# Kernel optimization log

Measured on AMD Instinct MI355X. Metric: run time of the kernel, lower is better.

## Reference

```python
import jax, jax.numpy as jnp
import numpy as np

CR = 64                      # cond_repeat
DILS = tuple(2 ** i for _ in range(2) for i in range(10))  # 2 blocks x 10 layers
Q_ZERO = 128


def setup_inputs() -> dict:
    key = jax.random.key(0)
    B, C, TE = 8, 64, 8          # batch, cond channels, encoding timesteps
    R, S, Q = 128, 128, 256      # residual, skip, classes
    L = len(DILS)
    ks = jax.random.split(key, 12)
    sc = 0.1
    return {
        "encodings": jax.random.normal(ks[0], (B, C, TE), jnp.float32),
        "first_w": jax.random.normal(ks[1], (R, 1, 2), jnp.float32) * sc,
        "first_b": jnp.zeros((R,), jnp.float32),
        "causal_w": jax.random.normal(ks[2], (L, 2 * R, R, 2), jnp.float32) * sc,
        "causal_b": jnp.zeros((L, 2 * R), jnp.float32),
        "cond_w": jax.random.normal(ks[3], (L, 2 * R, C), jnp.float32) * sc,
        "cond_b": jnp.zeros((L, 2 * R), jnp.float32),
        "res_w": jax.random.normal(ks[4], (L, R, R), jnp.float32) * sc,
        "res_b": jnp.zeros((L, R), jnp.float32),
        "skip_w": jax.random.normal(ks[5], (L, S, R), jnp.float32) * sc,
        "skip_b": jnp.zeros((L, S), jnp.float32),
        "skipc_w": jax.random.normal(ks[6], (S, R), jnp.float32) * sc,
        "skipc_b": jnp.zeros((S,), jnp.float32),
        "fc_w": jax.random.normal(ks[7], (S, S), jnp.float32) * sc,
        "fc_b": jnp.zeros((S,), jnp.float32),
        "condf_w": jax.random.normal(ks[8], (S, C), jnp.float32) * sc,
        "condf_b": jnp.zeros((S,), jnp.float32),
        "logits_w": jax.random.normal(ks[9], (Q, S), jnp.float32) * sc,
        "logits_b": jnp.zeros((Q,), jnp.float32),
    }


def _generate(encodings, first_w, first_b, causal_w, causal_b, cond_w, cond_b,
              res_w, res_b, skip_w, skip_b, skipc_w, skipc_b, fc_w, fc_b,
              condf_w, condf_b, logits_w, logits_b):
    B = encodings.shape[0]
    R = res_w.shape[1]
    T = encodings.shape[2] * CR

    # ring buffers emulate QueuedConv1d (queue length = dilation, zero-initialized)
    buf_first0 = jnp.zeros((B, 1), jnp.float32)
    bufs0 = tuple(jnp.zeros((B, d, R), jnp.float32) for d in DILS)
    sample0 = jnp.full((B,), Q_ZERO, jnp.int32)

    def step(carry, t):
        sample, buf_first, bufs = carry
        x = sample.astype(jnp.float32) / 255.0 - 0.5                      # [B]
        c = jax.lax.dynamic_index_in_dim(encodings, t // CR, axis=2,
                                         keepdims=False)                  # [B,C]
        # first causal conv (1 -> R, kernel 2): tap0 on delayed sample, tap1 on current
        prev0 = buf_first[:, 0]
        buf_first = buf_first.at[:, 0].set(x)
        res = (prev0[:, None] * first_w[None, :, 0, 0]
               + x[:, None] * first_w[None, :, 0, 1] + first_b)           # [B,R]
        skip = res @ skipc_w.T + skipc_b                                  # [B,S]
        new_bufs = []
        for l, d in enumerate(DILS):
            idx = jnp.mod(t, d)
            prev = jax.lax.dynamic_index_in_dim(bufs[l], idx, axis=1, keepdims=False)
            new_bufs.append(jax.lax.dynamic_update_index_in_dim(bufs[l], res, idx, axis=1))
            z = (prev @ causal_w[l, :, :, 0].T + res @ causal_w[l, :, :, 1].T
                 + causal_b[l] + c @ cond_w[l].T + cond_b[l])             # [B,2R]
            gate, out = jnp.split(z, 2, axis=1)
            h = jax.nn.sigmoid(gate) * jnp.tanh(out)                      # [B,R]
            res = res + h @ res_w[l].T + res_b[l]
            skip = skip + h @ skip_w[l].T + skip_b[l]
        s = jax.nn.relu(skip) @ fc_w.T + fc_b + c @ condf_w.T + condf_b
        logits = jax.nn.relu(s) @ logits_w.T + logits_b                   # [B,Q]
        sample = jnp.argmax(logits, axis=1).astype(jnp.int32)             # 'max' sampling
        return (sample, buf_first, tuple(new_bufs)), (sample, logits)

    _, (samples, logits) = jax.lax.scan(step, (sample0, buf_first0, bufs0),
                                        jnp.arange(T))
    return samples, logits  # [T,B] int32, [T,B,Q] float32


def reference(encodings, first_w, first_b, causal_w, causal_b, cond_w, cond_b,
              res_w, res_b, skip_w, skip_b, skipc_w, skipc_b, fc_w, fc_b,
              condf_w, condf_b, logits_w, logits_b):
    return _generate(encodings, first_w, first_b, causal_w, causal_b, cond_w, cond_b,
                     res_w, res_b, skip_w, skip_b, skipc_w, skipc_b, fc_w, fc_b,
                     condf_w, condf_b, logits_w, logits_b)
```

## Files before the change

### kernel.cpp

```cpp
#include <hip/hip_runtime.h>
#include <math.h>

#define BB 8
#define TT 512
#define LL 20
#define NBLK 64
#define NTHR 256

typedef float f4 __attribute__((ext_vector_type(4)));
typedef unsigned long long ull;

__constant__ int c_dil[LL] = {1,2,4,8,16,32,64,128,256,512,
                              1,2,4,8,16,32,64,128,256,512};
__constant__ int c_roff[LL] = {-1,0,4096,12288,28672,61440,126976,258048,520192,1044480,
                               2093056,2095104,2099200,2107392,2123776,2156544,
                               2222080,2353152,2615296,3139584};

constexpr size_t OFF_RING = 0;
constexpr size_t OFF_X    = 4188160;

#define P_WC     0
#define P_F      20480
#define P_WST    30208
#define P_WSKIPC 30720
#define P_WFC    30976
#define P_WLOG   31232
#define P_WF0    31744
#define P_WF1    31872
#define P_FB     32000
#define P_CONDZ  32128
#define P_SFC    32768
#define P_RESB   32784
#define P_SKIPB  32824
#define P_ZB     32864
#define P_LOGB   32944
#define P_SKIPCB 32948
#define P_Z0C    32952
#define P_SKC    32976
#define P_XS     32984
#define P_SZ     33008
#define P_SL     33040
#define P_SKACC  33072
#define P_R2     33088
#define P_CF     33104
#define P_PREVF  33632
#define P_HF     34688
#define P_RESF   35744
#define P_RES0   36800
#define POOL_FL  37856

__device__ __forceinline__ f4 ldx(const f4* p) {
    f4 r;
    asm volatile("global_load_dwordx4 %0, %1, off sc0 sc1\n\ts_waitcnt vmcnt(0)"
                 : "=v"(r) : "v"(p) : "memory");
    return r;
}
__device__ __forceinline__ void ldx2(const f4* p0, const f4* p1, f4& a, f4& b) {
    asm volatile("global_load_dwordx4 %0, %2, off sc0 sc1\n\t"
                 "global_load_dwordx4 %1, %3, off sc0 sc1\n\t"
                 "s_waitcnt vmcnt(0)"
                 : "=v"(a), "=v"(b) : "v"(p0), "v"(p1) : "memory");
}
__device__ __forceinline__ void ld4x(const f4* a0, const f4* a1, const f4* a2, const f4* a3,
                                     f4& r0, f4& r1, f4& r2, f4& r3) {
    asm volatile("global_load_dwordx4 %0, %4, off sc0 sc1\n\t"
                 "global_load_dwordx4 %1, %5, off sc0 sc1\n\t"
                 "global_load_dwordx4 %2, %6, off sc0 sc1\n\t"
                 "global_load_dwordx4 %3, %7, off sc0 sc1\n\t"
                 "s_waitcnt vmcnt(0)"
                 : "=v"(r0), "=v"(r1), "=v"(r2), "=v"(r3)
                 : "v"(a0), "v"(a1), "v"(a2), "v"(a3) : "memory");
}
__device__ __forceinline__ void stx(f4* p, f4 v) {
    asm volatile("global_store_dwordx4 %0, %1, off sc0 sc1"
                 :: "v"(p), "v"(v) : "memory");
}
__device__ __forceinline__ void spin(const f4* p, int e, f4& a) {
    while (__float_as_int(a.w) != e) a = ldx(p);
}

__device__ __forceinline__ float pick16(const float* sl, int V) {
    if (V < 8) return sl[V];
    if (V >= 9 && V < 17) return sl[V - 1];
    return 0.f;
}
__device__ __forceinline__ void publish16(f4* slot, int J, const float* sl, int e) {
    if (threadIdx.x < 6) {
        int q = threadIdx.x;
        f4 v;
        v.x = pick16(sl, 3*q);
        v.y = pick16(sl, 3*q + 1);
        v.z = pick16(sl, 3*q + 2);
        v.w = __int_as_float(e);
        stx(slot + J*6 + q, v);
    }
}
__device__ __forceinline__ void publish_half(f4* slot, int J, int r, const float* half8,
                                             int e, int m) {
    int base = 3*m;
    f4 v;
    v.x = half8[base];
    v.y = (base + 1 < 8) ? half8[base + 1] : 0.f;
    v.z = (base + 2 < 8) ? half8[base + 2] : 0.f;
    v.w = __int_as_float(e);
    stx(slot + J*6 + 3*r + m, v);
}
__device__ __forceinline__ void scat16(float* dst, f4 v, int vi, bool dorelu) {
    int j = vi / 6, q = vi - 6*j;
    #pragma unroll
    for (int i = 0; i < 3; ++i) {
        int V = 3*q + i;
        float x = v[i];
        if (dorelu) x = fmaxf(x, 0.f);
        if (V < 8)                 dst[V*132 + 2*j]           = x;
        else if (V >= 9 && V < 17) dst[(V - 9)*132 + 2*j + 1] = x;
    }
}
__device__ __forceinline__ void consume16(const f4* slot, int e, float* dst, bool dorelu) {
    int m = threadIdx.x;
    const f4 *p0 = slot + m, *p1 = slot + 256 + m;
    f4 a, b;
    bool two = (m < 128);
    if (two) ldx2(p0, p1, a, b); else a = ldx(p0);
    spin(p0, e, a);
    if (two) spin(p1, e, b);
    scat16(dst, a, m, dorelu);
    if (two) scat16(dst, b, m + 256, dorelu);
}
__device__ __forceinline__ void consume_pair(const f4* sR, int eR, float* dR,
                                             const f4* sH, int eH, float* dH) {
    int m = threadIdx.x;
    const f4 *pra = sR + m, *prb = sR + 256 + m, *pha = sH + m, *phb = sH + 256 + m;
    f4 ra, rb, ha, hb;
    bool two = (m < 128);
    if (two) ld4x(pra, prb, pha, phb, ra, rb, ha, hb);
    else     ldx2(pra, pha, ra, ha);
    spin(pra, eR, ra);
    if (two) spin(prb, eR, rb);
    scat16(dR, ra, m, false);
    if (two) scat16(dR, rb, m + 256, false);
    spin(pha, eH, ha);
    if (two) spin(phb, eH, hb);
    scat16(dH, ha, m, false);
    if (two) scat16(dH, hb, m + 256, false);
}

__global__ __launch_bounds__(NTHR, 1) void wn_gen(
    const float* __restrict__ enc,
    const float* __restrict__ first_w,  const float* __restrict__ first_b,
    const float* __restrict__ causal_w, const float* __restrict__ causal_b,
    const float* __restrict__ cond_w,   const float* __restrict__ cond_b,
    const float* __restrict__ res_w,    const float* __restrict__ res_b,
    const float* __restrict__ skip_w,   const float* __restrict__ skip_b,
    const float* __restrict__ skipc_w,  const float* __restrict__ skipc_b,
    const float* __restrict__ fc_w,     const float* __restrict__ fc_b,
    const float* __restrict__ condf_w,  const float* __restrict__ condf_b,
    const float* __restrict__ logits_w, const float* __restrict__ logits_b,
    float* __restrict__ wsf, float* __restrict__ out)
{
    extern __shared__ float pool[];
    const int tid = threadIdx.x;
    const int J = blockIdx.x;
    float* ring = wsf + OFF_RING;
    f4* xb = (f4*)(wsf + OFF_X);

    for (int m = tid; m < 20480; m += NTHR) {
        int l = m >> 10, rem = m & 1023, g = rem >> 8, i = rem & 255;
        int grow = (g < 2) ? (2*J + g) : (128 + 2*J + (g - 2));
        int col = i & 127, k = i >> 7;
        pool[P_WC + m] = causal_w[((size_t)(l*256 + grow)*128 + col)*2 + k];
    }
    if (tid < 256) {
        int r = tid >> 7, i = tid & 127;
        pool[P_WSKIPC + tid] = skipc_w[(size_t)(2*J + r)*128 + i];
        pool[P_WFC + tid]    = fc_w[(size_t)(2*J + r)*128 + i];
    }
    for (int m = tid; m < 512; m += NTHR) {
        int w = m >> 7, i = m & 127;
        pool[P_WLOG + m] = logits_w[(size_t)(4*J + w)*128 + i];
    }
    if (tid < 128) {
        pool[P_WF0 + tid] = first_w[2*tid];
        pool[P_WF1 + tid] = first_w[2*tid + 1];
        pool[P_FB + tid]  = first_b[tid];
    }
    if (tid < 40) {
        int l = tid >> 1, r = tid & 1;
        pool[P_RESB + tid]  = res_b[l*128 + 2*J + r];
        pool[P_SKIPB + tid] = skip_b[l*128 + 2*J + r];
    }
    if (tid < 4) pool[P_LOGB + tid] = logits_b[4*J + tid];
    if (tid < 2) pool[P_SKIPCB + tid] = skipc_b[2*J + tid];
    if (tid < 8) {
        pool[P_XS + tid]      = 128.f/255.f - 0.5f;
        pool[P_XS + 8 + tid]  = 0.f;
        pool[P_XS + 16 + tid] = 0.f;
    }
    __syncthreads();

    for (int l = 0; l < 19; ++l) {
        for (int m = tid; m < 512; m += NTHR) {
            int g = m >> 7, j = m & 127;
            const float* w1 = pool + P_WC + ((l+1)*4 + g)*256 + 128;
            const float* rw = res_w + (size_t)l*128*128 + j;
            float acc = 0.f;
            #pragma unroll 8
            for (int i = 0; i < 128; ++i) acc += w1[i] * rw[(size_t)i*128];
            pool[P_F + (l*4 + g)*128 + j] = acc;
        }
    }
    if (tid < 80) {
        int l = tid >> 2, g = tid & 3;
        float acc = 0.f;
        if (l >= 1) {
            const float* w1 = pool + P_WC + (l*4 + g)*256 + 128;
            for (int i = 0; i < 128; ++i) acc += w1[i] * res_b[(l-1)*128 + i];
        }
        pool[P_ZB + tid] = acc;
    }
    if (tid < 4) {
        const float* w0 = pool + P_WC + tid*256;
        const float* w1 = w0 + 128;
        float kp = 0.f, kc = 0.f, u = 0.f, c1 = 0.f, a0 = 0.f;
        for (int j = 0; j < 128; ++j) {
            float f0 = pool[P_WF0 + j], f1 = pool[P_WF1 + j], fbv = pool[P_FB + j];
            kp += w0[j]*fbv; kc += w1[j]*fbv;
            u  += w0[j]*f0;  c1 += w0[j]*f1 + w1[j]*f0;  a0 += w1[j]*f1;
        }
        pool[P_Z0C + tid*6 + 0] = kp;
        pool[P_Z0C + tid*6 + 1] = kc;
        pool[P_Z0C + tid*6 + 2] = u;
        pool[P_Z0C + tid*6 + 3] = c1;
        pool[P_Z0C + tid*6 + 4] = a0;
    }
    if (tid < 2) {
        const float* wr = pool + P_WSKIPC + tid*128;
        float sk = pool[P_SKIPCB + tid], sa = 0.f, sb = 0.f;
        for (int j = 0; j < 128; ++j) {
            sk += wr[j]*pool[P_FB + j];
            sa += wr[j]*pool[P_WF0 + j];
            sb += wr[j]*pool[P_WF1 + j];
        }
        pool[P_SKC + tid*3 + 0] = sk;
        pool[P_SKC + tid*3 + 1] = sa;
        pool[P_SKC + tid*3 + 2] = sb;
    }
    __syncthreads();

    int e = 0;
    int er_pending = 0;
    int esk = 0;

    for (int t = 0; t < TT; ++t) {
        if ((t & 63) == 0) {
            int te = t >> 6;
            for (int m = tid; m < 512; m += NTHR) {
                int b = m >> 6, j = m & 63;
                pool[P_CF + b*66 + j] = enc[(size_t)b*512 + j*8 + te];
            }
            __syncthreads();
            for (int m = tid; m < 640; m += NTHR) {
                int l = m >> 5, rem = m & 31, g = rem >> 3, b = rem & 7;
                int grow = (g < 2) ? (2*J + g) : (128 + 2*J + (g - 2));
                float acc = causal_b[l*256 + grow] + cond_b[l*256 + grow]
                          + pool[P_ZB + l*4 + g];
                const float* cw = cond_w + (size_t)(l*256 + grow)*64;
                const float* cf = pool + P_CF + b*66;
                for (int j = 0; j < 64; ++j) acc += cw[j]*cf[j];
                pool[P_CONDZ + l*32 + g*8 + b] = acc;
            }
            if (tid < 16) {
                int r = tid >> 3, b = tid & 7, row = 2*J + r;
                float acc = fc_b[row] + condf_b[row];
                const float* cw = condf_w + (size_t)row*64;
                const float* cf = pool + P_CF + b*66;
                for (int j = 0; j < 64; ++j) acc += cw[j]*cf[j];
                pool[P_SFC + r*8 + b] = acc;
            }
            __syncthreads();
        }

        ++e; const int eh0 = e;
        {
            if (tid < 16) {
                int r = tid & 1, b = tid >> 1;
                float kf  = (t >= 1) ? 1.f : 0.f;
                float x0v = pool[P_XS + b];
                float x1v = pool[P_XS + 8 + b];
                float x2v = pool[P_XS + 16 + b];
                const float* zc = pool + P_Z0C;
                int g0 = r, g1 = 2 + r;
                float zg = kf*zc[g0*6+0] + zc[g0*6+1] + x2v*zc[g0*6+2]
                         + x1v*zc[g0*6+3] + x0v*zc[g0*6+4] + pool[P_CONDZ + g0*8 + b];
                float zo = kf*zc[g1*6+0] + zc[g1*6+1] + x2v*zc[g1*6+2]
                         + x1v*zc[g1*6+3] + x0v*zc[g1*6+4] + pool[P_CONDZ + g1*8 + b];
                pool[P_SL + r*8 + b] = (1.f/(1.f + expf(-zg))) * tanhf(zo);
            }
            publish16(xb + (size_t)(eh0 & 3)*768, J, pool + P_SL, eh0);
        }
        for (int m = tid; m < 1024; m += NTHR) {
            int b = m >> 7, r = m & 127;
            pool[P_RES0 + b*132 + r] =
                pool[P_FB + r] + pool[P_XS + 8 + b]*pool[P_WF0 + r]
                               + pool[P_XS + b]    *pool[P_WF1 + r];
        }
        if (tid < 16) {
            int r = tid >> 3, b = tid & 7;
            float x0v = pool[P_XS + b], x1v = pool[P_XS + 8 + b];
            pool[P_SKACC + r*8 + b] = pool[P_SKC + r*3] + x1v*pool[P_SKC + r*3 + 1]
                                                        + x0v*pool[P_SKC + r*3 + 2];
            int row = 2*J + r;
            pool[P_R2 + r*8 + b] = pool[P_FB + row] + x1v*pool[P_WF0 + row]
                                                    + x0v*pool[P_WF1 + row];
        }

        for (int l = 0; l < LL; ++l) {
            int ehh;
            if (l == 0) {
                ehh = eh0;
            } else {
                {
                    int g = tid >> 6, lane = tid & 63, b = lane >> 3, k = lane & 7;
                    const float* w0 = pool + P_WC + (l*4 + g)*256;
                    const float* pv = pool + P_PREVF + b*132;
                    const float* rs = ((l == 1) ? pool + P_RES0 : pool + P_RESF) + b*132;
                    const float* fm = pool + P_F + ((l-1)*4 + g)*128;
                    const float* hh = pool + P_HF + b*132;
                    float acc = 0.f;
                    #pragma unroll
                    for (int i = 0; i < 16; ++i) {
                        int j = k + 8*i;
                        acc += w0[j]*pv[j] + w0[128 + j]*rs[j] + fm[j]*hh[j];
                    }
                    acc += __shfl_xor(acc,1); acc += __shfl_xor(acc,2); acc += __shfl_xor(acc,4);
                    if (k == 0) pool[P_SZ + g*8 + b] = acc;
                }
                __syncthreads();
                ++e; ehh = e;
                if (tid < 16) {
                    int r = tid & 1, b = tid >> 1;
                    float g = pool[P_SZ + r*8 + b]     + pool[P_CONDZ + l*32 + r*8 + b];
                    float o = pool[P_SZ + (2+r)*8 + b] + pool[P_CONDZ + l*32 + (2+r)*8 + b];
                    pool[P_SL + r*8 + b] = (1.f/(1.f + expf(-g))) * tanhf(o);
                }
                publish16(xb + (size_t)(ehh & 3)*768, J, pool + P_SL, ehh);
            }
            float wv0, wv1;
            {
                int r0 = tid >> 7, i0 = tid & 127;
                wv0 = res_w [(size_t)(l*128 + 2*J + r0)*128 + i0];
                wv1 = skip_w[(size_t)(l*128 + 2*J + r0)*128 + i0];
            }
            ull pfa = 0, pfb = 0;
            if (l <= 18) {
                int d = c_dil[l+1];
                if (t >= d) {
                    int slot = (t - d) & (2*d - 1);
                    const float* rp = ring + c_roff[l+1] + (size_t)slot*1024 + tid*4;
                    pfa = __hip_atomic_load((const ull*)rp,     __ATOMIC_RELAXED, __HIP_MEMORY_SCOPE_AGENT);
                    pfb = __hip_atomic_load((const ull*)(rp+2), __ATOMIC_RELAXED, __HIP_MEMORY_SCOPE_AGENT);
                }
            }
            if (l == 0) {
                consume16(xb + (size_t)(ehh & 3)*768, ehh, pool + P_HF, false);
            } else if (l <= 18) {
                consume_pair(xb + (size_t)(er_pending & 3)*768, er_pending, pool + P_RESF,
                             xb + (size_t)(ehh & 3)*768,        ehh,        pool + P_HF);
            } else {
                consume16(xb + (size_t)(ehh & 3)*768, ehh, pool + P_HF, false);
            }
            pool[P_WST + tid] = wv0;
            pool[P_WST + 256 + tid] = wv1;
            __syncthreads();
            {
                int w = tid >> 6, lane = tid & 63, b = lane >> 3, k = lane & 7;
                int r = w & 1, isSkip = w >> 1;
                if (isSkip || l <= 18) {
                    const float* wr = pool + P_WST + (isSkip ? 256 : 0) + r*128;
                    const float* hh = pool + P_HF + b*132;
                    float acc = 0.f;
                    #pragma unroll
                    for (int i = 0; i < 16; ++i) { int j = k + 8*i; acc += wr[j]*hh[j]; }
                    acc += __shfl_xor(acc,1); acc += __shfl_xor(acc,2); acc += __shfl_xor(acc,4);
                    if (k == 0) {
                        if (isSkip) {
                            pool[P_SKACC + r*8 + b] += acc + pool[P_SKIPB + l*2 + r];
                        } else {
                            float v = pool[P_R2 + r*8 + b] + acc + pool[P_RESB + l*2 + r];
                            pool[P_R2 + r*8 + b] = v;
                            pool[P_SL + r*8 + b] = v;
                            int d = c_dil[l+1];
                            int slot = t & (2*d - 1);
                            float* wp = ring + c_roff[l+1] + (size_t)slot*1024 + b*128 + 2*J + r;
                            __hip_atomic_store(wp, v, __ATOMIC_RELAXED, __HIP_MEMORY_SCOPE_AGENT);
                        }
                    }
                }
            }
            {
                int w = tid >> 6, lane = tid & 63;
                if (l <= 17) {
                    ++e; er_pending = e;
                    if (w < 2 && lane < 3)
                        publish_half(xb + (size_t)(e & 3)*768, J, w,
                                     pool + P_SL + w*8, e, lane);
                } else if (l == 19) {
                    ++e; esk = e;
                    if (w >= 2 && lane < 3)
                        publish_half(xb + (size_t)(e & 3)*768, J, w - 2,
                                     pool + P_SKACC + (w - 2)*8, e, lane);
                }
            }
            if (l <= 18) {
                int b = tid >> 5, c = (tid & 31)*4;
                union { ull u; float f[2]; } u0, u1;
                u0.u = pfa; u1.u = pfb;
                float* dp = pool + P_PREVF + b*132 + c;
                dp[0] = u0.f[0]; dp[1] = u0.f[1]; dp[2] = u1.f[0]; dp[3] = u1.f[1];
            }
            __syncthreads();
        }

        consume16(xb + (size_t)(esk & 3)*768, esk, pool + P_HF, false);
        __syncthreads();
        {
            int w = tid >> 6, lane = tid & 63, b = lane >> 3, k = lane & 7;
            if (w < 2) {
                const float* wr = pool + P_WFC + w*128;
                const float* sk = pool + P_HF + b*132;
                float acc = 0.f;
                #pragma unroll
                for (int i = 0; i < 16; ++i) { int j = k + 8*i; acc += wr[j]*fmaxf(sk[j], 0.f); }
                acc += __shfl_xor(acc,1); acc += __shfl_xor(acc,2); acc += __shfl_xor(acc,4);
                if (k == 0) pool[P_SL + w*8 + b] = acc + pool[P_SFC + w*8 + b];
            }
        }
        ++e;
        {
            int w = tid >> 6, lane = tid & 63;
            if (w < 2 && lane < 3)
                publish_half(xb + (size_t)(e & 3)*768, J, w, pool + P_SL + w*8, e, lane);
        }
        consume16(xb + (size_t)(e & 3)*768, e, pool + P_RESF, true);
        __syncthreads();
        {
            int b = tid >> 5, g = (tid >> 3) & 3, k = tid & 7;
            const float* wr = pool + P_WLOG + g*128;
            const float* sv = pool + P_RESF + b*132;
            float acc = 0.f;
            #pragma unroll
            for (int i = 0; i < 16; ++i) { int j = k + 8*i; acc += wr[j]*sv[j]; }
            acc += __shfl_xor(acc,1); acc += __shfl_xor(acc,2); acc += __shfl_xor(acc,4);
            float v = acc + pool[P_LOGB + g];
            float best = (k == 0) ? v : -3.4e38f;
            int bi = 4*J + g;
            { float ov = __shfl_xor(best, 8);  int oi = __shfl_xor(bi, 8);
              if (ov > best || (ov == best && oi < bi)) { best = ov; bi = oi; } }
            { float ov = __shfl_xor(best, 16); int oi = __shfl_xor(bi, 16);
              if (ov > best || (ov == best && oi < bi)) { best = ov; bi = oi; } }
            if (k == 0) out[4096 + ((size_t)(t*BB + b))*256 + 4*J + g] = v;
            if ((tid & 31) == 0) { pool[P_SL + b] = best; pool[P_SL + 8 + b] = (float)bi; }
        }
        __syncthreads();
        ++e;
        publish16(xb + (size_t)(e & 3)*768, J, pool + P_SL, e);
        consume16(xb + (size_t)(e & 3)*768, e, pool + P_HF, false);
        __syncthreads();
        if (tid < 64) {
            int b = tid >> 3, j0 = tid & 7;
            float best = -3.4e38f; float bidx = 0.f;
            #pragma unroll
            for (int k2 = 0; k2 < 8; ++k2) {
                int j = j0*8 + k2;
                float v  = pool[P_HF + b*132 + 2*j];
                float id = pool[P_HF + b*132 + 2*j + 1];
                if (v > best || (v == best && id < bidx)) { best = v; bidx = id; }
            }
            #pragma unroll
            for (int m = 4; m >= 1; m >>= 1) {
                float ov = __shfl_xor(best, m); float oi = __shfl_xor(bidx, m);
                if (ov > best || (ov == best && oi < bidx)) { best = ov; bidx = oi; }
            }
            if (j0 == 0) {
                if (J == 0) out[t*BB + b] = bidx;
                pool[P_XS + 16 + b] = pool[P_XS + 8 + b];
                pool[P_XS + 8 + b]  = pool[P_XS + b];
                pool[P_XS + b]      = bidx*(1.f/255.f) - 0.5f;
            }
        }
        __syncthreads();
    }
}

extern "C" void kernel_launch(void* const* d_in, const int* in_sizes, int n_in,
                              void* d_out, int out_size, void* d_ws, size_t ws_size,
                              hipStream_t stream) {
    const float* enc      = (const float*)d_in[0];
    const float* first_w  = (const float*)d_in[1];
    const float* first_b  = (const float*)d_in[2];
    const float* causal_w = (const float*)d_in[3];
    const float* causal_b = (const float*)d_in[4];
    const float* cond_w   = (const float*)d_in[5];
    const float* cond_b   = (const float*)d_in[6];
    const float* res_w    = (const float*)d_in[7];
    const float* res_b    = (const float*)d_in[8];
    const float* skip_w   = (const float*)d_in[9];
    const float* skip_b   = (const float*)d_in[10];
    const float* skipc_w  = (const float*)d_in[11];
    const float* skipc_b  = (const float*)d_in[12];
    const float* fc_w     = (const float*)d_in[13];
    const float* fc_b     = (const float*)d_in[14];
    const float* condf_w  = (const float*)d_in[15];
    const float* condf_b  = (const float*)d_in[16];
    const float* logits_w = (const float*)d_in[17];
    const float* logits_b = (const float*)d_in[18];

    float* wsf = (float*)d_ws;
    float* out = (float*)d_out;

    wn_gen<<<NBLK, NTHR, POOL_FL*4, stream>>>(
        enc, first_w, first_b, causal_w, causal_b, cond_w, cond_b,
        res_w, res_b, skip_w, skip_b, skipc_w, skipc_b, fc_w, fc_b,
        condf_w, condf_b, logits_w, logits_b, wsf, out);
}
```

Baseline: 35.99 ms.

## Compute layer-0 gate locally and fuse gate compute with publish to cut barriers

```diff
diff --git a/kernel.cpp b/kernel.cpp
--- a/kernel.cpp
+++ b/kernel.cpp
@@ -20,34 +20,30 @@
 constexpr size_t OFF_X    = 4188160;
 
 #define P_WC     0
+#define P_TB     0
 #define P_F      20480
-#define P_WST    30208
-#define P_WSKIPC 30720
-#define P_WFC    30976
-#define P_WLOG   31232
-#define P_WF0    31744
-#define P_WF1    31872
-#define P_FB     32000
-#define P_CONDZ  32128
-#define P_SFC    32768
-#define P_RESB   32784
-#define P_SKIPB  32824
-#define P_ZB     32864
-#define P_LOGB   32944
-#define P_SKIPCB 32948
-#define P_Z0C    32952
-#define P_SKC    32976
-#define P_XS     32984
-#define P_SZ     33008
-#define P_SL     33040
-#define P_SKACC  33072
-#define P_R2     33088
-#define P_CF     33104
-#define P_PREVF  33632
-#define P_HF     34688
-#define P_RESF   35744
-#define P_RES0   36800
-#define POOL_FL  37856
+#define P_CZ0    30208
+#define P_KC     32256
+#define P_WST    32512
+#define P_WF0    33024
+#define P_WF1    33152
+#define P_FB     33280
+#define P_CONDZ  33408
+#define P_SFC    34048
+#define P_RESB   34064
+#define P_SKIPB  34104
+#define P_ZB     34144
+#define P_LOGB   34224
+#define P_SKC    34228
+#define P_XS     34234
+#define P_SL     34258
+#define P_SKACC  34290
+#define P_R2     34306
+#define P_CF     34322
+#define P_PREVF  34852
+#define P_HF     35908
+#define P_RESF   38020
+#define POOL_FL  40132
 
 __device__ __forceinline__ f4 ldx(const f4* p) {
     f4 r;
@@ -59,7 +55,7 @@
     asm volatile("global_load_dwordx4 %0, %2, off sc0 sc1\n\t"
                  "global_load_dwordx4 %1, %3, off sc0 sc1\n\t"
                  "s_waitcnt vmcnt(0)"
-                 : "=v"(a), "=v"(b) : "v"(p0), "v"(p1) : "memory");
+                 : "=&v"(a), "=&v"(b) : "v"(p0), "v"(p1) : "memory");
 }
 __device__ __forceinline__ void ld4x(const f4* a0, const f4* a1, const f4* a2, const f4* a3,
                                      f4& r0, f4& r1, f4& r2, f4& r3) {
@@ -68,7 +64,7 @@
                  "global_load_dwordx4 %2, %6, off sc0 sc1\n\t"
                  "global_load_dwordx4 %3, %7, off sc0 sc1\n\t"
                  "s_waitcnt vmcnt(0)"
-                 : "=v"(r0), "=v"(r1), "=v"(r2), "=v"(r3)
+                 : "=&v"(r0), "=&v"(r1), "=&v"(r2), "=&v"(r3)
                  : "v"(a0), "v"(a1), "v"(a2), "v"(a3) : "memory");
 }
 __device__ __forceinline__ void stx(f4* p, f4 v) {
@@ -79,70 +75,46 @@
     while (__float_as_int(a.w) != e) a = ldx(p);
 }
 
-__device__ __forceinline__ float pick16(const float* sl, int V) {
-    if (V < 8) return sl[V];
-    if (V >= 9 && V < 17) return sl[V - 1];
-    return 0.f;
-}
-__device__ __forceinline__ void publish16(f4* slot, int J, const float* sl, int e) {
-    if (threadIdx.x < 6) {
-        int q = threadIdx.x;
-        f4 v;
-        v.x = pick16(sl, 3*q);
-        v.y = pick16(sl, 3*q + 1);
-        v.z = pick16(sl, 3*q + 2);
-        v.w = __int_as_float(e);
-        stx(slot + J*6 + q, v);
-    }
-}
-__device__ __forceinline__ void publish_half(f4* slot, int J, int r, const float* half8,
-                                             int e, int m) {
-    int base = 3*m;
-    f4 v;
-    v.x = half8[base];
-    v.y = (base + 1 < 8) ? half8[base + 1] : 0.f;
-    v.z = (base + 2 < 8) ? half8[base + 2] : 0.f;
-    v.w = __int_as_float(e);
-    stx(slot + J*6 + 3*r + m, v);
-}
-__device__ __forceinline__ void scat16(float* dst, f4 v, int vi, bool dorelu) {
-    int j = vi / 6, q = vi - 6*j;
-    #pragma unroll
-    for (int i = 0; i < 3; ++i) {
-        int V = 3*q + i;
-        float x = v[i];
-        if (dorelu) x = fmaxf(x, 0.f);
-        if (V < 8)                 dst[V*132 + 2*j]           = x;
-        else if (V >= 9 && V < 17) dst[(V - 9)*132 + 2*j + 1] = x;
-    }
-}
-__device__ __forceinline__ void consume16(const f4* slot, int e, float* dst, bool dorelu) {
+__device__ __forceinline__ void pub2(f4* slot, int J, int q, float v0, float v1, int e) {
+    f4 v; v.x = v0; v.y = v1; v.z = 0.f; v.w = __int_as_float(e);
+    stx(slot + J*8 + q, v);
+}
+__device__ __forceinline__ void scat2(float* dst, f4 v, int idx, bool dorelu) {
+    int Jb = idx >> 3, q = idx & 7;
+    float x = v.x, y = v.y;
+    if (dorelu) { x = fmaxf(x, 0.f); y = fmaxf(y, 0.f); }
+    if (q < 4) {
+        dst[(2*q)*132 + 2*Jb]     = x;
+        dst[(2*q+1)*132 + 2*Jb]   = y;
+    } else {
+        dst[(2*q-8)*132 + 2*Jb+1] = x;
+        dst[(2*q-7)*132 + 2*Jb+1] = y;
+    }
+}
+__device__ __forceinline__ void consume(const f4* slot, int e, float* dst, bool dorelu) {
     int m = threadIdx.x;
     const f4 *p0 = slot + m, *p1 = slot + 256 + m;
     f4 a, b;
-    bool two = (m < 128);
-    if (two) ldx2(p0, p1, a, b); else a = ldx(p0);
+    ldx2(p0, p1, a, b);
     spin(p0, e, a);
-    if (two) spin(p1, e, b);
-    scat16(dst, a, m, dorelu);
-    if (two) scat16(dst, b, m + 256, dorelu);
+    spin(p1, e, b);
+    scat2(dst, a, m, dorelu);
+    scat2(dst, b, m + 256, dorelu);
 }
 __device__ __forceinline__ void consume_pair(const f4* sR, int eR, float* dR,
                                              const f4* sH, int eH, float* dH) {
     int m = threadIdx.x;
     const f4 *pra = sR + m, *prb = sR + 256 + m, *pha = sH + m, *phb = sH + 256 + m;
     f4 ra, rb, ha, hb;
-    bool two = (m < 128);
-    if (two) ld4x(pra, prb, pha, phb, ra, rb, ha, hb);
-    else     ldx2(pra, pha, ra, ha);
+    ld4x(pra, prb, pha, phb, ra, rb, ha, hb);
     spin(pra, eR, ra);
-    if (two) spin(prb, eR, rb);
-    scat16(dR, ra, m, false);
-    if (two) scat16(dR, rb, m + 256, false);
+    spin(prb, eR, rb);
+    scat2(dR, ra, m, false);
+    scat2(dR, rb, m + 256, false);
     spin(pha, eH, ha);
-    if (two) spin(phb, eH, hb);
-    scat16(dH, ha, m, false);
-    if (two) scat16(dH, hb, m + 256, false);
+    spin(phb, eH, hb);
+    scat2(dH, ha, m, false);
+    scat2(dH, hb, m + 256, false);
 }
 
 __global__ __launch_bounds__(NTHR, 1) void wn_gen(
@@ -164,21 +136,12 @@
     float* ring = wsf + OFF_RING;
     f4* xb = (f4*)(wsf + OFF_X);
 
-    for (int m = tid; m < 20480; m += NTHR) {
+    for (int m = 1024 + tid; m < 20480; m += NTHR) {
         int l = m >> 10, rem = m & 1023, g = rem >> 8, i = rem & 255;
         int grow = (g < 2) ? (2*J + g) : (128 + 2*J + (g - 2));
         int col = i & 127, k = i >> 7;
         pool[P_WC + m] = causal_w[((size_t)(l*256 + grow)*128 + col)*2 + k];
     }
-    if (tid < 256) {
-        int r = tid >> 7, i = tid & 127;
-        pool[P_WSKIPC + tid] = skipc_w[(size_t)(2*J + r)*128 + i];
-        pool[P_WFC + tid]    = fc_w[(size_t)(2*J + r)*128 + i];
-    }
-    for (int m = tid; m < 512; m += NTHR) {
-        int w = m >> 7, i = m & 127;
-        pool[P_WLOG + m] = logits_w[(size_t)(4*J + w)*128 + i];
-    }
     if (tid < 128) {
         pool[P_WF0 + tid] = first_w[2*tid];
         pool[P_WF1 + tid] = first_w[2*tid + 1];
@@ -190,11 +153,21 @@
         pool[P_SKIPB + tid] = skip_b[l*128 + 2*J + r];
     }
     if (tid < 4) pool[P_LOGB + tid] = logits_b[4*J + tid];
-    if (tid < 2) pool[P_SKIPCB + tid] = skipc_b[2*J + tid];
     if (tid < 8) {
         pool[P_XS + tid]      = 128.f/255.f - 0.5f;
         pool[P_XS + 8 + tid]  = 0.f;
         pool[P_XS + 16 + tid] = 0.f;
+    }
+    float wl[16], wfc[16];
+    {
+        int g = (tid >> 3) & 3, k = tid & 7;
+        #pragma unroll
+        for (int i = 0; i < 16; ++i)
+            wl[i] = logits_w[(size_t)(4*J + g)*128 + k + 8*i];
+        int r2 = (tid >> 6) & 1;
+        #pragma unroll
+        for (int i = 0; i < 16; ++i)
+            wfc[i] = fc_w[(size_t)(2*J + r2)*128 + k + 8*i];
     }
     __syncthreads();
 
@@ -218,24 +191,25 @@
         }
         pool[P_ZB + tid] = acc;
     }
-    if (tid < 4) {
-        const float* w0 = pool + P_WC + tid*256;
-        const float* w1 = w0 + 128;
-        float kp = 0.f, kc = 0.f, u = 0.f, c1 = 0.f, a0 = 0.f;
+    {
+        int grow = tid;
+        const float* cw0 = causal_w + (size_t)grow*256;
+        float u = 0.f, c1 = 0.f, a0 = 0.f, kp = 0.f, kc = 0.f;
         for (int j = 0; j < 128; ++j) {
+            float w0 = cw0[2*j], w1 = cw0[2*j + 1];
             float f0 = pool[P_WF0 + j], f1 = pool[P_WF1 + j], fbv = pool[P_FB + j];
-            kp += w0[j]*fbv; kc += w1[j]*fbv;
-            u  += w0[j]*f0;  c1 += w0[j]*f1 + w1[j]*f0;  a0 += w1[j]*f1;
-        }
-        pool[P_Z0C + tid*6 + 0] = kp;
-        pool[P_Z0C + tid*6 + 1] = kc;
-        pool[P_Z0C + tid*6 + 2] = u;
-        pool[P_Z0C + tid*6 + 3] = c1;
-        pool[P_Z0C + tid*6 + 4] = a0;
+            u  += w0*f0;  c1 += w0*f1 + w1*f0;  a0 += w1*f1;
+            kp += w0*fbv; kc += w1*fbv;
+        }
+        pool[P_TB + grow*4 + 0] = u;
+        pool[P_TB + grow*4 + 1] = c1;
+        pool[P_TB + grow*4 + 2] = a0;
+        pool[P_TB + grow*4 + 3] = kp;
+        pool[P_KC + grow]       = kc;
     }
     if (tid < 2) {
-        const float* wr = pool + P_WSKIPC + tid*128;
-        float sk = pool[P_SKIPCB + tid], sa = 0.f, sb = 0.f;
+        const float* wr = skipc_w + (size_t)(2*J + tid)*128;
+        float sk = skipc_b[2*J + tid], sa = 0.f, sb = 0.f;
         for (int j = 0; j < 128; ++j) {
             sk += wr[j]*pool[P_FB + j];
             sa += wr[j]*pool[P_WF0 + j];
@@ -250,6 +224,8 @@
     int e = 0;
     int er_pending = 0;
     int esk = 0;
+
+    const int w = tid >> 6, lane = tid & 63;
 
     for (int t = 0; t < TT; ++t) {
         if ((t & 63) == 0) {
@@ -269,6 +245,17 @@
                 for (int j = 0; j < 64; ++j) acc += cw[j]*cf[j];
                 pool[P_CONDZ + l*32 + g*8 + b] = acc;
             }
+            {
+                int grow = tid;
+                float base = pool[P_KC + grow] + causal_b[grow] + cond_b[grow];
+                const float* cw = cond_w + (size_t)grow*64;
+                for (int b = 0; b < 8; ++b) {
+                    const float* cf = pool + P_CF + b*66;
+                    float acc = base;
+                    for (int j = 0; j < 64; ++j) acc += cw[j]*cf[j];
+                    pool[P_CZ0 + grow*8 + b] = acc;
+                }
+            }
             if (tid < 16) {
                 int r = tid >> 3, b = tid & 7, row = 2*J + r;
                 float acc = fc_b[row] + condf_b[row];
@@ -280,27 +267,25 @@
             __syncthreads();
         }
 
-        ++e; const int eh0 = e;
         {
-            if (tid < 16) {
-                int r = tid & 1, b = tid >> 1;
-                float kf  = (t >= 1) ? 1.f : 0.f;
-                float x0v = pool[P_XS + b];
-                float x1v = pool[P_XS + 8 + b];
-                float x2v = pool[P_XS + 16 + b];
-                const float* zc = pool + P_Z0C;
-                int g0 = r, g1 = 2 + r;
-                float zg = kf*zc[g0*6+0] + zc[g0*6+1] + x2v*zc[g0*6+2]
-                         + x1v*zc[g0*6+3] + x0v*zc[g0*6+4] + pool[P_CONDZ + g0*8 + b];
-                float zo = kf*zc[g1*6+0] + zc[g1*6+1] + x2v*zc[g1*6+2]
-                         + x1v*zc[g1*6+3] + x0v*zc[g1*6+4] + pool[P_CONDZ + g1*8 + b];
-                pool[P_SL + r*8 + b] = (1.f/(1.f + expf(-zg))) * tanhf(zo);
-            }
-            publish16(xb + (size_t)(eh0 & 3)*768, J, pool + P_SL, eh0);
+            int j = tid & 127, bh2 = tid >> 7;
+            float kf = (t >= 1) ? 1.f : 0.f;
+            const float* tg = pool + P_TB + j*4;
+            const float* to = pool + P_TB + (128 + j)*4;
+            #pragma unroll
+            for (int bb = 0; bb < 4; ++bb) {
+                int b = bh2*4 + bb;
+                float x0v = pool[P_XS + b], x1v = pool[P_XS + 8 + b], x2v = pool[P_XS + 16 + b];
+                float zg = pool[P_CZ0 + j*8 + b]
+                         + x2v*tg[0] + x1v*tg[1] + x0v*tg[2] + kf*tg[3];
+                float zo = pool[P_CZ0 + (128 + j)*8 + b]
+                         + x2v*to[0] + x1v*to[1] + x0v*to[2] + kf*to[3];
+                pool[P_HF + b*132 + j] = (1.f/(1.f + expf(-zg))) * tanhf(zo);
+            }
         }
         for (int m = tid; m < 1024; m += NTHR) {
             int b = m >> 7, r = m & 127;
-            pool[P_RES0 + b*132 + r] =
+            pool[P_RESF + b*132 + r] =
                 pool[P_FB + r] + pool[P_XS + 8 + b]*pool[P_WF0 + r]
                                + pool[P_XS + b]    *pool[P_WF1 + r];
         }
@@ -315,35 +300,34 @@
         }
 
         for (int l = 0; l < LL; ++l) {
-            int ehh;
-            if (l == 0) {
-                ehh = eh0;
-            } else {
-                {
-                    int g = tid >> 6, lane = tid & 63, b = lane >> 3, k = lane & 7;
-                    const float* w0 = pool + P_WC + (l*4 + g)*256;
-                    const float* pv = pool + P_PREVF + b*132;
-                    const float* rs = ((l == 1) ? pool + P_RES0 : pool + P_RESF) + b*132;
-                    const float* fm = pool + P_F + ((l-1)*4 + g)*128;
-                    const float* hh = pool + P_HF + b*132;
-                    float acc = 0.f;
-                    #pragma unroll
-                    for (int i = 0; i < 16; ++i) {
-                        int j = k + 8*i;
-                        acc += w0[j]*pv[j] + w0[128 + j]*rs[j] + fm[j]*hh[j];
-                    }
-                    acc += __shfl_xor(acc,1); acc += __shfl_xor(acc,2); acc += __shfl_xor(acc,4);
-                    if (k == 0) pool[P_SZ + g*8 + b] = acc;
+            const int par = l & 1;
+            int ehh = 0;
+            if (l >= 1) {
+                ++e; ehh = e;
+                const int r = w & 1, bh = w >> 1;
+                const int b2 = lane >> 4, half = (lane >> 3) & 1, k = lane & 7;
+                const int b = bh*4 + b2, g = half*2 + r;
+                const float* wz = pool + P_WC + (l*4 + g)*256;
+                const float* fm = pool + P_F + ((l-1)*4 + g)*128;
+                const float* pv = pool + P_PREVF + b*132;
+                const float* rs = pool + P_RESF + (par^1)*1056 + b*132;
+                const float* hh = pool + P_HF + (par^1)*1056 + b*132;
+                float acc = 0.f;
+                #pragma unroll
+                for (int i = 0; i < 16; ++i) {
+                    int j = k + 8*i;
+                    acc += wz[j]*pv[j] + wz[128 + j]*rs[j] + fm[j]*hh[j];
                 }
-                __syncthreads();
-                ++e; ehh = e;
-                if (tid < 16) {
-                    int r = tid & 1, b = tid >> 1;
-                    float g = pool[P_SZ + r*8 + b]     + pool[P_CONDZ + l*32 + r*8 + b];
-                    float o = pool[P_SZ + (2+r)*8 + b] + pool[P_CONDZ + l*32 + (2+r)*8 + b];
-                    pool[P_SL + r*8 + b] = (1.f/(1.f + expf(-g))) * tanhf(o);
-                }
-                publish16(xb + (size_t)(ehh & 3)*768, J, pool + P_SL, ehh);
+                acc += __shfl_xor(acc,1); acc += __shfl_xor(acc,2); acc += __shfl_xor(acc,4);
+                acc += pool[P_CONDZ + l*32 + g*8 + b];
+                float zp = __shfl_xor(acc, 8);
+                float zg = half ? zp : acc;
+                float zo = half ? acc : zp;
+                float h  = (1.f/(1.f + expf(-zg))) * tanhf(zo);
+                float hnb = __shfl_xor(h, 16);
+                if (half == 0 && k == 0 && (b2 & 1) == 0)
+                    pub2(xb + (size_t)(ehh & 3)*512, J,
+                         r*4 + bh*2 + (b2 >> 1), h, hnb, ehh);
             }
             float wv0, wv1;
             {
@@ -361,56 +345,56 @@
                     pfb = __hip_atomic_load((const ull*)(rp+2), __ATOMIC_RELAXED, __HIP_MEMORY_SCOPE_AGENT);
                 }
             }
-            if (l == 0) {
-                consume16(xb + (size_t)(ehh & 3)*768, ehh, pool + P_HF, false);
-            } else if (l <= 18) {
-                consume_pair(xb + (size_t)(er_pending & 3)*768, er_pending, pool + P_RESF,
-                             xb + (size_t)(ehh & 3)*768,        ehh,        pool + P_HF);
-            } else {
-                consume16(xb + (size_t)(ehh & 3)*768, ehh, pool + P_HF, false);
+            if (l >= 1 && l <= 18) {
+                consume_pair(xb + (size_t)(er_pending & 3)*512, er_pending,
+                             pool + P_RESF + par*1056,
+                             xb + (size_t)(ehh & 3)*512, ehh,
+                             pool + P_HF + par*1056);
+            } else if (l == 19) {
+                consume(xb + (size_t)(ehh & 3)*512, ehh, pool + P_HF + par*1056, false);
             }
             pool[P_WST + tid] = wv0;
             pool[P_WST + 256 + tid] = wv1;
             __syncthreads();
             {
-                int w = tid >> 6, lane = tid & 63, b = lane >> 3, k = lane & 7;
+                int b = lane >> 3, k = lane & 7;
                 int r = w & 1, isSkip = w >> 1;
                 if (isSkip || l <= 18) {
                     const float* wr = pool + P_WST + (isSkip ? 256 : 0) + r*128;
-                    const float* hh = pool + P_HF + b*132;
+                    const float* hh = pool + P_HF + par*1056 + b*132;
                     float acc = 0.f;
                     #pragma unroll
                     for (int i = 0; i < 16; ++i) { int j = k + 8*i; acc += wr[j]*hh[j]; }
                     acc += __shfl_xor(acc,1); acc += __shfl_xor(acc,2); acc += __shfl_xor(acc,4);
-                    if (k == 0) {
-                        if (isSkip) {
-                            pool[P_SKACC + r*8 + b] += acc + pool[P_SKIPB + l*2 + r];
-                        } else {
-                            float v = pool[P_R2 + r*8 + b] + acc + pool[P_RESB + l*2 + r];
+                    if (isSkip) {
+                        float v = pool[P_SKACC + r*8 + b] + acc + pool[P_SKIPB + l*2 + r];
+                        if (k == 0) pool[P_SKACC + r*8 + b] = v;
+                        if (l == 19) {
+                            float vnb = __shfl_xor(v, 8);
+                            if (k == 0 && !(b & 1))
+                                pub2(xb + (size_t)((e+1) & 3)*512, J,
+                                     r*4 + (b >> 1), v, vnb, e + 1);
+                        }
+                    } else {
+                        float v = pool[P_R2 + r*8 + b] + acc + pool[P_RESB + l*2 + r];
+                        if (k == 0) {
                             pool[P_R2 + r*8 + b] = v;
-                            pool[P_SL + r*8 + b] = v;
                             int d = c_dil[l+1];
                             int slot = t & (2*d - 1);
                             float* wp = ring + c_roff[l+1] + (size_t)slot*1024 + b*128 + 2*J + r;
                             __hip_atomic_store(wp, v, __ATOMIC_RELAXED, __HIP_MEMORY_SCOPE_AGENT);
                         }
+                        if (l <= 17) {
+                            float vnb = __shfl_xor(v, 8);
+                            if (k == 0 && !(b & 1))
+                                pub2(xb + (size_t)((e+1) & 3)*512, J,
+                                     r*4 + (b >> 1), v, vnb, e + 1);
+                        }
                     }
                 }
             }
-            {
-                int w = tid >> 6, lane = tid & 63;
-                if (l <= 17) {
-                    ++e; er_pending = e;
-                    if (w < 2 && lane < 3)
-                        publish_half(xb + (size_t)(e & 3)*768, J, w,
-                                     pool + P_SL + w*8, e, lane);
-                } else if (l == 19) {
-                    ++e; esk = e;
-                    if (w >= 2 && lane < 3)
-                        publish_half(xb + (size_t)(e & 3)*768, J, w - 2,
-                                     pool + P_SKACC + (w - 2)*8, e, lane);
-                }
-            }
+            if (l <= 17)      { ++e; er_pending = e; }
+            else if (l == 19) { ++e; esk = e; }
             if (l <= 18) {
                 int b = tid >> 5, c = (tid & 31)*4;
                 union { ull u; float f[2]; } u0, u1;
@@ -421,35 +405,31 @@
             __syncthreads();
         }
 
-        consume16(xb + (size_t)(esk & 3)*768, esk, pool + P_HF, false);
+        consume(xb + (size_t)(esk & 3)*512, esk, pool + P_HF, false);
         __syncthreads();
+        ++e;
         {
-            int w = tid >> 6, lane = tid & 63, b = lane >> 3, k = lane & 7;
+            int b = lane >> 3, k = lane & 7, r = w & 1;
             if (w < 2) {
-                const float* wr = pool + P_WFC + w*128;
                 const float* sk = pool + P_HF + b*132;
                 float acc = 0.f;
                 #pragma unroll
-                for (int i = 0; i < 16; ++i) { int j = k + 8*i; acc += wr[j]*fmaxf(sk[j], 0.f); }
+                for (int i = 0; i < 16; ++i) { int j = k + 8*i; acc += wfc[i]*fmaxf(sk[j], 0.f); }
                 acc += __shfl_xor(acc,1); acc += __shfl_xor(acc,2); acc += __shfl_xor(acc,4);
-                if (k == 0) pool[P_SL + w*8 + b] = acc + pool[P_SFC + w*8 + b];
-            }
-        }
-        ++e;
-        {
-            int w = tid >> 6, lane = tid & 63;
-            if (w < 2 && lane < 3)
-                publish_half(xb + (size_t)(e & 3)*768, J, w, pool + P_SL + w*8, e, lane);
-        }
-        consume16(xb + (size_t)(e & 3)*768, e, pool + P_RESF, true);
+                float v = acc + pool[P_SFC + r*8 + b];
+                float vnb = __shfl_xor(v, 8);
+                if (k == 0 && !(b & 1))
+                    pub2(xb + (size_t)(e & 3)*512, J, r*4 + (b >> 1), v, vnb, e);
+            }
+        }
+        consume(xb + (size_t)(e & 3)*512, e, pool + P_RESF, true);
         __syncthreads();
         {
             int b = tid >> 5, g = (tid >> 3) & 3, k = tid & 7;
-            const float* wr = pool + P_WLOG + g*128;
             const float* sv = pool + P_RESF + b*132;
             float acc = 0.f;
             #pragma unroll
-            for (int i = 0; i < 16; ++i) { int j = k + 8*i; acc += wr[j]*sv[j]; }
+            for (int i = 0; i < 16; ++i) { int j = k + 8*i; acc += wl[i]*sv[j]; }
             acc += __shfl_xor(acc,1); acc += __shfl_xor(acc,2); acc += __shfl_xor(acc,4);
             float v = acc + pool[P_LOGB + g];
             float best = (k == 0) ? v : -3.4e38f;
@@ -459,12 +439,18 @@
             { float ov = __shfl_xor(best, 16); int oi = __shfl_xor(bi, 16);
               if (ov > best || (ov == best && oi < bi)) { best = ov; bi = oi; } }
             if (k == 0) out[4096 + ((size_t)(t*BB + b))*256 + 4*J + g] = v;
-            if ((tid & 31) == 0) { pool[P_SL + b] = best; pool[P_SL + 8 + b] = (float)bi; }
+            if ((tid & 31) == 0) { pool[P_SL + 2*b] = best; pool[P_SL + 2*b + 1] = (float)bi; }
         }
         __syncthreads();
         ++e;
-        publish16(xb + (size_t)(e & 3)*768, J, pool + P_SL, e);
-        consume16(xb + (size_t)(e & 3)*768, e, pool + P_HF, false);
+        if (tid < 8) {
+            int q = tid;
+            float v0, v1;
+            if (q < 4) { v0 = pool[P_SL + 4*q];     v1 = pool[P_SL + 4*q + 2]; }
+            else       { v0 = pool[P_SL + 4*(q-4) + 1]; v1 = pool[P_SL + 4*(q-4) + 3]; }
+            pub2(xb + (size_t)(e & 3)*512, J, q, v0, v1, e);
+        }
+        consume(xb + (size_t)(e & 3)*512, e, pool + P_HF, false);
         __syncthreads();
         if (tid < 64) {
             int b = tid >> 3, j0 = tid & 7;
```

Measured after the change: 37.01 ms. 1.03x slower.
